# Optimization experiments

Hardware: AMD Instinct MI355X
Metric: run time of the kernel (lower is better)

Reference implementation:

```python
import jax, jax.numpy as jnp
import numpy as np

N_SAMPLES = 8192
EMBED_DIM = 128
NUM_CLASSES = 100


def setup_inputs() -> dict:
    key = jax.random.key(0)
    k1, k2 = jax.random.split(key)
    x = jax.random.normal(k1, (N_SAMPLES, EMBED_DIM), dtype=jnp.float32)
    # FastAP assumes L2-normalized embeddings (dist2 = 2 - 2*cos in [0, 4])
    x = x / jnp.linalg.norm(x, axis=1, keepdims=True)
    labels = jax.random.randint(k2, (N_SAMPLES,), 0, NUM_CLASSES, dtype=jnp.int64 if jax.config.jax_enable_x64 else jnp.int32)
    return {"batch": x, "labels": labels, "num_bins": 10}


def reference(batch, labels, num_bins):
    N = batch.shape[0]
    L = num_bins + 1                      # number of histogram bin centers (edges of linspace)
    Delta = 4.0 / num_bins                # bin width
    Z = jnp.linspace(0.0, 4.0, L)

    same = labels[:, None] == labels[None, :]
    eye = jnp.eye(N, dtype=bool)
    I_pos = (same & ~eye).astype(batch.dtype)   # Aff > 0
    I_neg = (~same).astype(batch.dtype)         # Aff < 0 (diag is 'same', so excluded)
    N_pos = I_pos.sum(axis=1)

    # squared euclidean distance for unit-norm rows: 2 - 2*cos
    dist2 = 2.0 - 2.0 * (batch @ batch.T)       # [N, N]

    # soft-binning histogram: one N x N pulse per bin, reduced to per-row counts.
    # lax.map keeps only one [N, N] pulse buffer alive at a time.
    def bin_fn(z):
        pulse = jnp.maximum(0.0, 1.0 - jnp.abs(dist2 - z) / Delta)
        return (jnp.einsum('ij,ij->i', pulse, I_pos),
                jnp.einsum('ij,ij->i', pulse, I_neg))

    hp, hn = jax.lax.map(bin_fn, Z)             # each [L, N]
    h_pos = hp.T                                # [N, L]
    h_neg = hn.T

    H_pos = jnp.cumsum(h_pos, axis=1)
    H = jnp.cumsum(h_pos + h_neg, axis=1)

    # FastAP = h_pos * H_pos / H, with NaN/Inf (H == 0) zeroed, as in the original
    safe_H = jnp.where(H > 0, H, 1.0)
    ap = jnp.where(H > 0, h_pos * H_pos / safe_H, 0.0).sum(axis=1)

    # divide by N_pos; rows with no positives are dropped from the mean
    valid = N_pos > 0
    safe_Np = jnp.where(valid, N_pos, 1.0)
    ap = jnp.where(valid, ap / safe_Np, 0.0)

    n_valid = valid.sum().astype(batch.dtype)
    loss = 1.0 - ap.sum() / n_valid
    return loss
```

## Files before the change

kernel.cpp:

```cpp
#include <hip/hip_runtime.h>

#define NS 8192
#define EMBED 128
#define ROWCHUNK 512
#define NPANEL (ROWCHUNK / 32)
#define AROW 12
#define INV64K (1.0f / 65536.0f)

typedef __bf16 bf16x8 __attribute__((ext_vector_type(8)));
typedef float f32x4 __attribute__((ext_vector_type(4)));
typedef float f32x2 __attribute__((ext_vector_type(2)));
typedef const __attribute__((address_space(1))) unsigned ag_u32;
typedef __attribute__((address_space(3))) unsigned al_u32;

#define OFF_XB  0u
#define OFF_GS  2097152u
#define OFF_GSP 2228224u
#define OFF_GA  2359296u
#define OFF_GAP 2752512u
#define OFF_CC  3145728u
#define OFF_AC  3146240u
#define ZERO_BYTES 1049120u

__device__ inline unsigned short f2bf(float f) {
  unsigned u = __float_as_uint(f);
  u += 0x7fffu + ((u >> 16) & 1u);
  return (unsigned short)(u >> 16);
}
__device__ inline float clamp01(float x) { return __builtin_amdgcn_fmed3f(x, 0.f, 1.f); }
__device__ inline f32x2 pkclamp01(f32x2 v) {
  return __builtin_elementwise_min(__builtin_elementwise_max(v, (f32x2){0.f, 0.f}),
                                   (f32x2){1.f, 1.f});
}

__global__ __launch_bounds__(256) void prep_kernel(const float* __restrict__ x,
                                                   unsigned short* __restrict__ xb,
                                                   uint4* __restrict__ zbase) {
  const int gid = blockIdx.x * 256 + threadIdx.x;
  const int row = gid >> 4, g = gid & 15;
  const float4 v0 = reinterpret_cast<const float4*>(x)[row * 32 + g * 2];
  const float4 v1 = reinterpret_cast<const float4*>(x)[row * 32 + g * 2 + 1];
  uint4 o;
  o.x = (unsigned)f2bf(v0.x) | ((unsigned)f2bf(v0.y) << 16);
  o.y = (unsigned)f2bf(v0.z) | ((unsigned)f2bf(v0.w) << 16);
  o.z = (unsigned)f2bf(v1.x) | ((unsigned)f2bf(v1.y) << 16);
  o.w = (unsigned)f2bf(v1.z) | ((unsigned)f2bf(v1.w) << 16);
  reinterpret_cast<uint4*>(xb)[row * 16 + (g ^ (row & 7))] = o;
  if (gid < (int)(ZERO_BYTES / 16u)) zbase[gid] = make_uint4(0u, 0u, 0u, 0u);
}

__global__ __launch_bounds__(256, 8) void fastap_main_kernel(
    const unsigned short* __restrict__ xb,
    const int* __restrict__ labels,
    unsigned* __restrict__ gS, unsigned* __restrict__ gSp,
    unsigned* __restrict__ gA, unsigned* __restrict__ gAp,
    int* __restrict__ ccount) {
  __shared__ __align__(16) unsigned short sA[2][32 * 128];
  __shared__ int sLab[ROWCHUNK];

  const int tid  = threadIdx.x;
  const int wave = tid >> 6;
  const int lane = tid & 63;
  const int l16  = lane & 15;
  const int quad = lane >> 4;
  const int colBase  = blockIdx.x * 64;
  const int rowChunk = blockIdx.y * ROWCHUNK;

  if (tid < ROWCHUNK / 4)
    reinterpret_cast<int4*>(sLab)[tid] =
        reinterpret_cast<const int4*>(labels + rowChunk)[tid];

  const int jcol = colBase + wave * 16 + l16;
  bf16x8 bfr[4];
  #pragma unroll
  for (int kb = 0; kb < 4; ++kb) {
    const int pg = (kb * 4 + quad) ^ (l16 & 7);
    bfr[kb] = *reinterpret_cast<const bf16x8*>(&xb[jcol * 128 + pg * 8]);
  }
  const int labj = labels[jcol];

  f32x2 C01 = {0.f, 0.f}, C23 = {0.f, 0.f};
  f32x2 Cp01 = {0.f, 0.f}, Cp23 = {0.f, 0.f};

  int aOff[4];
  #pragma unroll
  for (int kb = 0; kb < 4; ++kb)
    aOff[kb] = l16 * 128 + (((kb * 4 + quad) ^ (l16 & 7)) << 3);

  const unsigned short* xrb = xb + rowChunk * 128;
  auto stage = [&](int p, int b) {
    const unsigned short* src = xrb + p * (32 * 128);
    __builtin_amdgcn_global_load_lds((ag_u32*)(src + tid * 8),
                                     (al_u32*)(&sA[b][tid * 8]), 16, 0, 0);
    __builtin_amdgcn_global_load_lds((ag_u32*)(src + (tid + 256) * 8),
                                     (al_u32*)(&sA[b][(tid + 256) * 8]), 16, 0, 0);
  };

  auto tile16 = [&](const unsigned short* ap, int lcr) {
    const int4 lr = *reinterpret_cast<const int4*>(&sLab[lcr + quad * 4]);
    bf16x8 a0 = *reinterpret_cast<const bf16x8*>(&ap[aOff[0]]);
    bf16x8 a1 = *reinterpret_cast<const bf16x8*>(&ap[aOff[1]]);
    bf16x8 a2 = *reinterpret_cast<const bf16x8*>(&ap[aOff[2]]);
    bf16x8 a3 = *reinterpret_cast<const bf16x8*>(&ap[aOff[3]]);
    f32x4 acc = {0.f, 0.f, 0.f, 0.f};
    acc = __builtin_amdgcn_mfma_f32_16x16x32_bf16(a0, bfr[0], acc, 0, 0, 0);
    acc = __builtin_amdgcn_mfma_f32_16x16x32_bf16(a1, bfr[1], acc, 0, 0, 0);
    acc = __builtin_amdgcn_mfma_f32_16x16x32_bf16(a2, bfr[2], acc, 0, 0, 0);
    acc = __builtin_amdgcn_mfma_f32_16x16x32_bf16(a3, bfr[3], acc, 0, 0, 0);

    const int labr[4] = {lr.x, lr.y, lr.z, lr.w};
    #pragma unroll
    for (int r = 0; r < 4; ++r) {
      const float a = acc[r];
      const float pm = (labr[r] == labj) ? 1.f : 0.f;
      const f32x2 av = {a, a}, p2 = {pm, pm};
      const f32x2 d01 = pkclamp01(__builtin_elementwise_fma(av, (f32x2){5.f, 5.f},
                                                            (f32x2){-1.f, 0.f}));
      const f32x2 d23 = pkclamp01(__builtin_elementwise_fma(av, (f32x2){5.f, 5.f},
                                                            (f32x2){1.f, 2.f}));
      C01 += d01; C23 += d23;
      Cp01 = __builtin_elementwise_fma(p2, d01, Cp01);
      Cp23 = __builtin_elementwise_fma(p2, d23, Cp23);
    }

    const float mabs = fmaxf(fmaxf(fabsf(acc[0]), fabsf(acc[1])),
                             fmaxf(fabsf(acc[2]), fabsf(acc[3])));
    if (__builtin_expect(mabs > 0.4f, 0)) {
      #pragma unroll
      for (int r = 0; r < 4; ++r) {
        const float a = acc[r];
        if (fabsf(a) <= 0.4f) continue;
        const int i = rowChunk + lcr + quad * 4 + r;
        const float d0 = clamp01(fmaf(a, 5.f, -1.f));
        const float d1 = clamp01(a * 5.f);
        const float d2 = clamp01(fmaf(a, 5.f, 1.f));
        const float d3 = clamp01(fmaf(a, 5.f, 2.f));
        if (i == jcol) {
          C01 -= (f32x2){d0, d1};  C23 -= (f32x2){d2, d3};
          Cp01 -= (f32x2){d0, d1}; Cp23 -= (f32x2){d2, d3};
          #pragma unroll
          for (int k = 7; k <= 10; ++k)
            atomicAdd(&gA[jcol * AROW + k], (unsigned)(-65536));
        } else {
          const bool isPos = (labr[r] == labj);
          const float t = fmaf(a, -5.f, 5.f);
          #pragma unroll
          for (int k = 0; k <= 2; ++k) {
            const float v = clamp01((float)(k + 1) - t);
            const int q = (int)(v * 65536.f + 0.5f);
            if (q) {
              atomicAdd(&gA[jcol * AROW + k], (unsigned)q);
              if (isPos) atomicAdd(&gAp[jcol * AROW + k], (unsigned)q);
            }
          }
          #pragma unroll
          for (int k = 7; k <= 10; ++k) {
            const float v = clamp01((float)(k + 1) - t) - 1.f;
            const int q = (int)(v * 65536.f - 0.5f);
            if (q) {
              atomicAdd(&gA[jcol * AROW + k], (unsigned)q);
              if (isPos) atomicAdd(&gAp[jcol * AROW + k], (unsigned)q);
            }
          }
        }
      }
    }
  };

  stage(0, 0);
  __syncthreads();

  if (blockIdx.x == 0) {
    for (int idx = tid; idx < ROWCHUNK; idx += 256)
      atomicAdd(&ccount[sLab[idx]], 1);
  }

  #pragma unroll 1
  for (int p = 0; p < NPANEL; ++p) {
    const int cur = p & 1;
    if (p + 1 < NPANEL) stage(p + 1, cur ^ 1);
    tile16(&sA[cur][0],        p * 32);
    tile16(&sA[cur][16 * 128], p * 32 + 16);
    __syncthreads();
  }

  #pragma unroll
  for (int m = 16; m < 64; m <<= 1) {
    C01.x  += __shfl_xor(C01.x,  m, 64); C01.y  += __shfl_xor(C01.y,  m, 64);
    C23.x  += __shfl_xor(C23.x,  m, 64); C23.y  += __shfl_xor(C23.y,  m, 64);
    Cp01.x += __shfl_xor(Cp01.x, m, 64); Cp01.y += __shfl_xor(Cp01.y, m, 64);
    Cp23.x += __shfl_xor(Cp23.x, m, 64); Cp23.y += __shfl_xor(Cp23.y, m, 64);
  }

  if (quad == 0) {
    const float Cv[4]  = {C01.x, C01.y, C23.x, C23.y};
    const float Cpv[4] = {Cp01.x, Cp01.y, Cp23.x, Cp23.y};
    #pragma unroll
    for (int k = 0; k < 4; ++k) {
      atomicAdd(&gS[jcol * 4 + k],  (unsigned)(int)lrintf(Cv[k]  * 65536.f));
      atomicAdd(&gSp[jcol * 4 + k], (unsigned)(int)lrintf(Cpv[k] * 65536.f));
    }
  }
}

__global__ __launch_bounds__(256) void epilogue_kernel(
    const unsigned* __restrict__ gS, const unsigned* __restrict__ gSp,
    const unsigned* __restrict__ gA, const unsigned* __restrict__ gAp,
    const int* __restrict__ labels, const int* __restrict__ ccount,
    float* __restrict__ accum, unsigned* __restrict__ done,
    float* __restrict__ out) {
  const int i = blockIdx.x * 256 + threadIdx.x;
  const int np = ccount[labels[i]] - 1;
  float ap = 0.f, val = 0.f, HpPrev = 0.f;
  #pragma unroll
  for (int b = 0; b <= 10; ++b) {
    const float baseH  = (b < 3) ? 0.f
                       : (b < 7) ? (float)(int)gS[i * 4 + (b - 3)]  * INV64K : 8192.f;
    const float basePp = (b < 3) ? 0.f
                       : (b < 7) ? (float)(int)gSp[i * 4 + (b - 3)] * INV64K : (float)np;
    const float H  = baseH  + (float)(int)gA[i * AROW + b]  * INV64K;
    const float Hp = basePp + (float)(int)gAp[i * AROW + b] * INV64K;
    const float hp = Hp - HpPrev;
    HpPrev = Hp;
    if (H > 1e-6f) ap += hp * Hp / H;
  }
  if (np > 0) { ap /= (float)np; val = 1.f; } else ap = 0.f;

  __shared__ float sa[256], sv[256];
  sa[threadIdx.x] = ap; sv[threadIdx.x] = val;
  __syncthreads();
  for (int s = 128; s > 0; s >>= 1) {
    if (threadIdx.x < s) {
      sa[threadIdx.x] += sa[threadIdx.x + s];
      sv[threadIdx.x] += sv[threadIdx.x + s];
    }
    __syncthreads();
  }
  if (threadIdx.x == 0) {
    atomicAdd(&accum[0], sa[0]);
    atomicAdd(&accum[1], sv[0]);
    __threadfence();
    const unsigned prev = atomicAdd(done, 1u);
    if (prev == gridDim.x - 1) {
      const float a = atomicAdd(&accum[0], 0.f);
      const float c = atomicAdd(&accum[1], 0.f);
      out[0] = 1.f - (c > 0.f ? a / c : 0.f);
    }
  }
}

extern "C" void kernel_launch(void* const* d_in, const int* in_sizes, int n_in,
                              void* d_out, int out_size, void* d_ws, size_t ws_size,
                              hipStream_t stream) {
  const float* x      = (const float*)d_in[0];
  const int*   labels = (const int*)d_in[1];
  float* out = (float*)d_out;

  char* ws = (char*)d_ws;
  unsigned short* xb = (unsigned short*)(ws + OFF_XB);
  unsigned* gS   = (unsigned*)(ws + OFF_GS);
  unsigned* gSp  = (unsigned*)(ws + OFF_GSP);
  unsigned* gA   = (unsigned*)(ws + OFF_GA);
  unsigned* gAp  = (unsigned*)(ws + OFF_GAP);
  int*      cc   = (int*)(ws + OFF_CC);
  float*    accum = (float*)(ws + OFF_AC);
  unsigned* done  = (unsigned*)(ws + OFF_AC + 8);

  prep_kernel<<<512, 256, 0, stream>>>(x, xb, (uint4*)(ws + OFF_GS));
  fastap_main_kernel<<<dim3(NS / 64, NS / ROWCHUNK), 256, 0, stream>>>(
      xb, labels, gS, gSp, gA, gAp, cc);
  epilogue_kernel<<<NS / 256, 256, 0, stream>>>(gS, gSp, gA, gAp, labels, cc,
                                                accum, done, out);
}
```

Before: 113.0 us.

## Share A fragments across two column subtiles and replace sum atomics with partial buffers

Each wave now computes a 16x32 tile per panel: one set of LDS A-fragments feeds MFMAs for two 16-column subtiles, which halves LDS reads per MFMA and puts two independent accumulator chains in flight. The per-column bin sums gS/gSp are no longer fixed-point atomics. Each (row-chunk, wave-row) slot writes plain float4 partials, and the epilogue reduces the 32 slots, so that region no longer needs zeroing. The positive-mask FMA is skipped when no lane in the wave has a positive. The cost is higher register pressure (occupancy hint lowered from 8 to 4), a larger workspace, and extra epilogue reads.

```diff
diff --git a/kernel.cpp b/kernel.cpp
--- a/kernel.cpp
+++ b/kernel.cpp
@@ -15,12 +15,12 @@
 
 #define OFF_XB  0u
 #define OFF_GS  2097152u
-#define OFF_GSP 2228224u
-#define OFF_GA  2359296u
-#define OFF_GAP 2752512u
-#define OFF_CC  3145728u
-#define OFF_AC  3146240u
-#define ZERO_BYTES 1049120u
+#define OFF_GSP 6291456u
+#define OFF_GA  10485760u
+#define OFF_GAP 10878976u
+#define OFF_CC  11272192u
+#define OFF_AC  11272704u
+#define ZERO_BYTES 786960u
 
 __device__ inline unsigned short f2bf(float f) {
   unsigned u = __float_as_uint(f);
@@ -28,10 +28,6 @@
   return (unsigned short)(u >> 16);
 }
 __device__ inline float clamp01(float x) { return __builtin_amdgcn_fmed3f(x, 0.f, 1.f); }
-__device__ inline f32x2 pkclamp01(f32x2 v) {
-  return __builtin_elementwise_min(__builtin_elementwise_max(v, (f32x2){0.f, 0.f}),
-                                   (f32x2){1.f, 1.f});
-}
 
 __global__ __launch_bounds__(256) void prep_kernel(const float* __restrict__ x,
                                                    unsigned short* __restrict__ xb,
@@ -49,10 +45,10 @@
   if (gid < (int)(ZERO_BYTES / 16u)) zbase[gid] = make_uint4(0u, 0u, 0u, 0u);
 }
 
-__global__ __launch_bounds__(256, 8) void fastap_main_kernel(
+__global__ __launch_bounds__(256, 4) void fastap_main_kernel(
     const unsigned short* __restrict__ xb,
     const int* __restrict__ labels,
-    unsigned* __restrict__ gS, unsigned* __restrict__ gSp,
+    float* __restrict__ gS, float* __restrict__ gSp,
     unsigned* __restrict__ gA, unsigned* __restrict__ gAp,
     int* __restrict__ ccount) {
   __shared__ __align__(16) unsigned short sA[2][32 * 128];
@@ -63,6 +59,8 @@
   const int lane = tid & 63;
   const int l16  = lane & 15;
   const int quad = lane >> 4;
+  const int w2   = wave >> 1;
+  const int wr   = wave & 1;
   const int colBase  = blockIdx.x * 64;
   const int rowChunk = blockIdx.y * ROWCHUNK;
 
@@ -70,22 +68,31 @@
     reinterpret_cast<int4*>(sLab)[tid] =
         reinterpret_cast<const int4*>(labels + rowChunk)[tid];
 
-  const int jcol = colBase + wave * 16 + l16;
-  bf16x8 bfr[4];
-  #pragma unroll
-  for (int kb = 0; kb < 4; ++kb) {
-    const int pg = (kb * 4 + quad) ^ (l16 & 7);
-    bfr[kb] = *reinterpret_cast<const bf16x8*>(&xb[jcol * 128 + pg * 8]);
-  }
-  const int labj = labels[jcol];
-
-  f32x2 C01 = {0.f, 0.f}, C23 = {0.f, 0.f};
-  f32x2 Cp01 = {0.f, 0.f}, Cp23 = {0.f, 0.f};
+  bf16x8 bfr[2][4];
+  int jcolv[2], labj[2];
+  #pragma unroll
+  for (int s = 0; s < 2; ++s) {
+    const int jc = colBase + w2 * 32 + s * 16 + l16;
+    jcolv[s] = jc;
+    labj[s] = labels[jc];
+    #pragma unroll
+    for (int kb = 0; kb < 4; ++kb) {
+      const int pg = (kb * 4 + quad) ^ (l16 & 7);
+      bfr[s][kb] = *reinterpret_cast<const bf16x8*>(&xb[jc * 128 + pg * 8]);
+    }
+  }
+
+  f32x2 C01[2], C23[2], Cp01[2], Cp23[2];
+  #pragma unroll
+  for (int s = 0; s < 2; ++s) {
+    C01[s] = (f32x2){0.f, 0.f};  C23[s] = (f32x2){0.f, 0.f};
+    Cp01[s] = (f32x2){0.f, 0.f}; Cp23[s] = (f32x2){0.f, 0.f};
+  }
 
   int aOff[4];
   #pragma unroll
   for (int kb = 0; kb < 4; ++kb)
-    aOff[kb] = l16 * 128 + (((kb * 4 + quad) ^ (l16 & 7)) << 3);
+    aOff[kb] = (wr * 16 + l16) * 128 + (((kb * 4 + quad) ^ (l16 & 7)) << 3);
 
   const unsigned short* xrb = xb + rowChunk * 128;
   auto stage = [&](int p, int b) {
@@ -96,70 +103,88 @@
                                      (al_u32*)(&sA[b][(tid + 256) * 8]), 16, 0, 0);
   };
 
-  auto tile16 = [&](const unsigned short* ap, int lcr) {
-    const int4 lr = *reinterpret_cast<const int4*>(&sLab[lcr + quad * 4]);
+  auto panel = [&](const unsigned short* ap, int p) {
+    const int4 lr = *reinterpret_cast<const int4*>(&sLab[p * 32 + wr * 16 + quad * 4]);
     bf16x8 a0 = *reinterpret_cast<const bf16x8*>(&ap[aOff[0]]);
     bf16x8 a1 = *reinterpret_cast<const bf16x8*>(&ap[aOff[1]]);
     bf16x8 a2 = *reinterpret_cast<const bf16x8*>(&ap[aOff[2]]);
     bf16x8 a3 = *reinterpret_cast<const bf16x8*>(&ap[aOff[3]]);
-    f32x4 acc = {0.f, 0.f, 0.f, 0.f};
-    acc = __builtin_amdgcn_mfma_f32_16x16x32_bf16(a0, bfr[0], acc, 0, 0, 0);
-    acc = __builtin_amdgcn_mfma_f32_16x16x32_bf16(a1, bfr[1], acc, 0, 0, 0);
-    acc = __builtin_amdgcn_mfma_f32_16x16x32_bf16(a2, bfr[2], acc, 0, 0, 0);
-    acc = __builtin_amdgcn_mfma_f32_16x16x32_bf16(a3, bfr[3], acc, 0, 0, 0);
+    f32x4 acc0 = {0.f, 0.f, 0.f, 0.f};
+    f32x4 acc1 = {0.f, 0.f, 0.f, 0.f};
+    acc0 = __builtin_amdgcn_mfma_f32_16x16x32_bf16(a0, bfr[0][0], acc0, 0, 0, 0);
+    acc1 = __builtin_amdgcn_mfma_f32_16x16x32_bf16(a0, bfr[1][0], acc1, 0, 0, 0);
+    acc0 = __builtin_amdgcn_mfma_f32_16x16x32_bf16(a1, bfr[0][1], acc0, 0, 0, 0);
+    acc1 = __builtin_amdgcn_mfma_f32_16x16x32_bf16(a1, bfr[1][1], acc1, 0, 0, 0);
+    acc0 = __builtin_amdgcn_mfma_f32_16x16x32_bf16(a2, bfr[0][2], acc0, 0, 0, 0);
+    acc1 = __builtin_amdgcn_mfma_f32_16x16x32_bf16(a2, bfr[1][2], acc1, 0, 0, 0);
+    acc0 = __builtin_amdgcn_mfma_f32_16x16x32_bf16(a3, bfr[0][3], acc0, 0, 0, 0);
+    acc1 = __builtin_amdgcn_mfma_f32_16x16x32_bf16(a3, bfr[1][3], acc1, 0, 0, 0);
 
     const int labr[4] = {lr.x, lr.y, lr.z, lr.w};
     #pragma unroll
     for (int r = 0; r < 4; ++r) {
-      const float a = acc[r];
-      const float pm = (labr[r] == labj) ? 1.f : 0.f;
-      const f32x2 av = {a, a}, p2 = {pm, pm};
-      const f32x2 d01 = pkclamp01(__builtin_elementwise_fma(av, (f32x2){5.f, 5.f},
-                                                            (f32x2){-1.f, 0.f}));
-      const f32x2 d23 = pkclamp01(__builtin_elementwise_fma(av, (f32x2){5.f, 5.f},
-                                                            (f32x2){1.f, 2.f}));
-      C01 += d01; C23 += d23;
-      Cp01 = __builtin_elementwise_fma(p2, d01, Cp01);
-      Cp23 = __builtin_elementwise_fma(p2, d23, Cp23);
-    }
-
-    const float mabs = fmaxf(fmaxf(fabsf(acc[0]), fabsf(acc[1])),
-                             fmaxf(fabsf(acc[2]), fabsf(acc[3])));
-    if (__builtin_expect(mabs > 0.4f, 0)) {
       #pragma unroll
-      for (int r = 0; r < 4; ++r) {
-        const float a = acc[r];
-        if (fabsf(a) <= 0.4f) continue;
-        const int i = rowChunk + lcr + quad * 4 + r;
-        const float d0 = clamp01(fmaf(a, 5.f, -1.f));
-        const float d1 = clamp01(a * 5.f);
-        const float d2 = clamp01(fmaf(a, 5.f, 1.f));
-        const float d3 = clamp01(fmaf(a, 5.f, 2.f));
-        if (i == jcol) {
-          C01 -= (f32x2){d0, d1};  C23 -= (f32x2){d2, d3};
-          Cp01 -= (f32x2){d0, d1}; Cp23 -= (f32x2){d2, d3};
-          #pragma unroll
-          for (int k = 7; k <= 10; ++k)
-            atomicAdd(&gA[jcol * AROW + k], (unsigned)(-65536));
-        } else {
-          const bool isPos = (labr[r] == labj);
-          const float t = fmaf(a, -5.f, 5.f);
-          #pragma unroll
-          for (int k = 0; k <= 2; ++k) {
-            const float v = clamp01((float)(k + 1) - t);
-            const int q = (int)(v * 65536.f + 0.5f);
-            if (q) {
-              atomicAdd(&gA[jcol * AROW + k], (unsigned)q);
-              if (isPos) atomicAdd(&gAp[jcol * AROW + k], (unsigned)q);
+      for (int s = 0; s < 2; ++s) {
+        const float a = (s == 0) ? acc0[r] : acc1[r];
+        const f32x2 av = {a, a};
+        f32x2 d01 = __builtin_elementwise_fma(av, (f32x2){5.f, 5.f}, (f32x2){-1.f, 0.f});
+        f32x2 d23 = __builtin_elementwise_fma(av, (f32x2){5.f, 5.f}, (f32x2){1.f, 2.f});
+        d01 = (f32x2){clamp01(d01.x), clamp01(d01.y)};
+        d23 = (f32x2){clamp01(d23.x), clamp01(d23.y)};
+        C01[s] += d01; C23[s] += d23;
+        const bool isPos = (labr[r] == labj[s]);
+        if (__any(isPos)) {
+          const float pm = isPos ? 1.f : 0.f;
+          const f32x2 p2 = {pm, pm};
+          Cp01[s] = __builtin_elementwise_fma(p2, d01, Cp01[s]);
+          Cp23[s] = __builtin_elementwise_fma(p2, d23, Cp23[s]);
+        }
+      }
+    }
+
+    const float m0 = fmaxf(fmaxf(fabsf(acc0[0]), fabsf(acc0[1])),
+                           fmaxf(fabsf(acc0[2]), fabsf(acc0[3])));
+    const float m1 = fmaxf(fmaxf(fabsf(acc1[0]), fabsf(acc1[1])),
+                           fmaxf(fabsf(acc1[2]), fabsf(acc1[3])));
+    if (__builtin_expect(fmaxf(m0, m1) > 0.4f, 0)) {
+      #pragma unroll
+      for (int s = 0; s < 2; ++s) {
+        #pragma unroll
+        for (int r = 0; r < 4; ++r) {
+          const float a = (s == 0) ? acc0[r] : acc1[r];
+          if (fabsf(a) <= 0.4f) continue;
+          const int i = rowChunk + p * 32 + wr * 16 + quad * 4 + r;
+          const int jc = jcolv[s];
+          const float d0 = clamp01(fmaf(a, 5.f, -1.f));
+          const float d1 = clamp01(a * 5.f);
+          const float d2 = clamp01(fmaf(a, 5.f, 1.f));
+          const float d3 = clamp01(fmaf(a, 5.f, 2.f));
+          if (i == jc) {
+            C01[s] -= (f32x2){d0, d1};  C23[s] -= (f32x2){d2, d3};
+            Cp01[s] -= (f32x2){d0, d1}; Cp23[s] -= (f32x2){d2, d3};
+            #pragma unroll
+            for (int k = 7; k <= 10; ++k)
+              atomicAdd(&gA[jc * AROW + k], (unsigned)(-65536));
+          } else {
+            const bool isPos = (labr[r] == labj[s]);
+            const float t = fmaf(a, -5.f, 5.f);
+            #pragma unroll
+            for (int k = 0; k <= 2; ++k) {
+              const float v = clamp01((float)(k + 1) - t);
+              const int q = (int)(v * 65536.f + 0.5f);
+              if (q) {
+                atomicAdd(&gA[jc * AROW + k], (unsigned)q);
+                if (isPos) atomicAdd(&gAp[jc * AROW + k], (unsigned)q);
+              }
             }
-          }
-          #pragma unroll
-          for (int k = 7; k <= 10; ++k) {
-            const float v = clamp01((float)(k + 1) - t) - 1.f;
-            const int q = (int)(v * 65536.f - 0.5f);
-            if (q) {
-              atomicAdd(&gA[jcol * AROW + k], (unsigned)q);
-              if (isPos) atomicAdd(&gAp[jcol * AROW + k], (unsigned)q);
+            #pragma unroll
+            for (int k = 7; k <= 10; ++k) {
+              const float v = clamp01((float)(k + 1) - t) - 1.f;
+              const int q = (int)(v * 65536.f - 0.5f);
+              if (q) {
+                atomicAdd(&gA[jc * AROW + k], (unsigned)q);
+                if (isPos) atomicAdd(&gAp[jc * AROW + k], (unsigned)q);
+              }
             }
           }
         }
@@ -179,45 +204,60 @@
   for (int p = 0; p < NPANEL; ++p) {
     const int cur = p & 1;
     if (p + 1 < NPANEL) stage(p + 1, cur ^ 1);
-    tile16(&sA[cur][0],        p * 32);
-    tile16(&sA[cur][16 * 128], p * 32 + 16);
+    panel(&sA[cur][0], p);
     __syncthreads();
   }
 
   #pragma unroll
   for (int m = 16; m < 64; m <<= 1) {
-    C01.x  += __shfl_xor(C01.x,  m, 64); C01.y  += __shfl_xor(C01.y,  m, 64);
-    C23.x  += __shfl_xor(C23.x,  m, 64); C23.y  += __shfl_xor(C23.y,  m, 64);
-    Cp01.x += __shfl_xor(Cp01.x, m, 64); Cp01.y += __shfl_xor(Cp01.y, m, 64);
-    Cp23.x += __shfl_xor(Cp23.x, m, 64); Cp23.y += __shfl_xor(Cp23.y, m, 64);
+    #pragma unroll
+    for (int s = 0; s < 2; ++s) {
+      C01[s].x  += __shfl_xor(C01[s].x,  m, 64); C01[s].y  += __shfl_xor(C01[s].y,  m, 64);
+      C23[s].x  += __shfl_xor(C23[s].x,  m, 64); C23[s].y  += __shfl_xor(C23[s].y,  m, 64);
+      Cp01[s].x += __shfl_xor(Cp01[s].x, m, 64); Cp01[s].y += __shfl_xor(Cp01[s].y, m, 64);
+      Cp23[s].x += __shfl_xor(Cp23[s].x, m, 64); Cp23[s].y += __shfl_xor(Cp23[s].y, m, 64);
+    }
   }
 
   if (quad == 0) {
-    const float Cv[4]  = {C01.x, C01.y, C23.x, C23.y};
-    const float Cpv[4] = {Cp01.x, Cp01.y, Cp23.x, Cp23.y};
+    const int slot = blockIdx.y * 2 + wr;
     #pragma unroll
-    for (int k = 0; k < 4; ++k) {
-      atomicAdd(&gS[jcol * 4 + k],  (unsigned)(int)lrintf(Cv[k]  * 65536.f));
-      atomicAdd(&gSp[jcol * 4 + k], (unsigned)(int)lrintf(Cpv[k] * 65536.f));
+    for (int s = 0; s < 2; ++s) {
+      const float4 cv  = make_float4(C01[s].x,  C01[s].y,  C23[s].x,  C23[s].y);
+      const float4 cpv = make_float4(Cp01[s].x, Cp01[s].y, Cp23[s].x, Cp23[s].y);
+      reinterpret_cast<float4*>(gS)[slot * NS + jcolv[s]]  = cv;
+      reinterpret_cast<float4*>(gSp)[slot * NS + jcolv[s]] = cpv;
     }
   }
 }
 
 __global__ __launch_bounds__(256) void epilogue_kernel(
-    const unsigned* __restrict__ gS, const unsigned* __restrict__ gSp,
+    const float* __restrict__ gS, const float* __restrict__ gSp,
     const unsigned* __restrict__ gA, const unsigned* __restrict__ gAp,
     const int* __restrict__ labels, const int* __restrict__ ccount,
     float* __restrict__ accum, unsigned* __restrict__ done,
     float* __restrict__ out) {
   const int i = blockIdx.x * 256 + threadIdx.x;
   const int np = ccount[labels[i]] - 1;
+  const float4* gS4  = reinterpret_cast<const float4*>(gS);
+  const float4* gSp4 = reinterpret_cast<const float4*>(gSp);
+  float4 Cs  = make_float4(0.f, 0.f, 0.f, 0.f);
+  float4 Cps = make_float4(0.f, 0.f, 0.f, 0.f);
+  #pragma unroll 8
+  for (int c = 0; c < 32; ++c) {
+    const float4 u = gS4[c * NS + i];
+    const float4 v = gSp4[c * NS + i];
+    Cs.x += u.x; Cs.y += u.y; Cs.z += u.z; Cs.w += u.w;
+    Cps.x += v.x; Cps.y += v.y; Cps.z += v.z; Cps.w += v.w;
+  }
+  const float CsA[4]  = {Cs.x, Cs.y, Cs.z, Cs.w};
+  const float CpsA[4] = {Cps.x, Cps.y, Cps.z, Cps.w};
+
   float ap = 0.f, val = 0.f, HpPrev = 0.f;
   #pragma unroll
   for (int b = 0; b <= 10; ++b) {
-    const float baseH  = (b < 3) ? 0.f
-                       : (b < 7) ? (float)(int)gS[i * 4 + (b - 3)]  * INV64K : 8192.f;
-    const float basePp = (b < 3) ? 0.f
-                       : (b < 7) ? (float)(int)gSp[i * 4 + (b - 3)] * INV64K : (float)np;
+    const float baseH  = (b < 3) ? 0.f : (b < 7) ? CsA[b - 3]  : 8192.f;
+    const float basePp = (b < 3) ? 0.f : (b < 7) ? CpsA[b - 3] : (float)np;
     const float H  = baseH  + (float)(int)gA[i * AROW + b]  * INV64K;
     const float Hp = basePp + (float)(int)gAp[i * AROW + b] * INV64K;
     const float hp = Hp - HpPrev;
@@ -258,15 +298,15 @@
 
   char* ws = (char*)d_ws;
   unsigned short* xb = (unsigned short*)(ws + OFF_XB);
-  unsigned* gS   = (unsigned*)(ws + OFF_GS);
-  unsigned* gSp  = (unsigned*)(ws + OFF_GSP);
+  float*    gS   = (float*)(ws + OFF_GS);
+  float*    gSp  = (float*)(ws + OFF_GSP);
   unsigned* gA   = (unsigned*)(ws + OFF_GA);
   unsigned* gAp  = (unsigned*)(ws + OFF_GAP);
   int*      cc   = (int*)(ws + OFF_CC);
   float*    accum = (float*)(ws + OFF_AC);
   unsigned* done  = (unsigned*)(ws + OFF_AC + 8);
 
-  prep_kernel<<<512, 256, 0, stream>>>(x, xb, (uint4*)(ws + OFF_GS));
+  prep_kernel<<<512, 256, 0, stream>>>(x, xb, (uint4*)(ws + OFF_GA));
   fastap_main_kernel<<<dim3(NS / 64, NS / ROWCHUNK), 256, 0, stream>>>(
       xb, labels, gS, gSp, gA, gAp, cc);
   epilogue_kernel<<<NS / 256, 256, 0, stream>>>(gS, gSp, gA, gAp, labels, cc,
```

Result: slower. 118.3 us (+4.7%).
